# Performance work log

Hardware: AMD Instinct MI355X
Metric: run time of the kernel (lower is better)

The kernel has to match this reference:

```python
import jax, jax.numpy as jnp
import numpy as np

N, H, T, L, D_IN, D_QK, D_V = 8, 8, 1024, 1024, 128, 128, 128


def setup_inputs() -> dict:
    key = jax.random.key(0)
    ks = jax.random.split(key, 12)
    s = 1.0 / np.sqrt(D_IN)
    sq = 1.0 / np.sqrt(D_QK)
    return {
        "X": jax.random.normal(ks[0], (N, H, L, D_IN), jnp.float32),
        "t1": jax.random.normal(ks[1], (N, T), jnp.float32),
        "Q": jax.random.normal(ks[2], (N, H, T, D_QK), jnp.float32),
        "Wk1": jax.random.normal(ks[3], (D_IN, D_QK), jnp.float32) * s,
        "bk1": jnp.zeros((D_QK,), jnp.float32),
        "Wk2": jax.random.normal(ks[4], (D_QK, D_QK), jnp.float32) * sq,
        "bk2": jnp.zeros((D_QK,), jnp.float32),
        "Wv1": jax.random.normal(ks[5], (D_IN, D_QK), jnp.float32) * s,
        "bv1": jnp.zeros((D_QK,), jnp.float32),
        "Wv2": jax.random.normal(ks[6], (D_QK, D_V), jnp.float32) * sq,
        "bv2": jnp.zeros((D_V,), jnp.float32),
        "log_tau": jnp.asarray(0.0, jnp.float32),  # log(init_tau=1)
    }


def _mlp(x, W1, b1, W2, b2):
    # MLP(d_in, [d_qk], d_out): Linear -> relu -> Linear
    return jax.nn.relu(x @ W1 + b1) @ W2 + b2


def reference(X, t1, Q, Wk1, bk1, Wk2, bk2, Wv1, bv1, Wv2, bv2, log_tau):
    t2 = X[:, 0, :, -1]                      # (N, L)
    K = _mlp(X, Wk1, bk1, Wk2, bk2)          # (N, H, L, d_qk)
    V = _mlp(X, Wv1, bv1, Wv2, bv2)          # (N, H, L, d_v)
    tau = jnp.exp(log_tau)
    # gaussian weight: -(Q.K)^2 / tau
    A = jnp.einsum('nhtc,nhlc->nhtl', Q, K)
    A = -(A * A) / tau
    mask = (t1[:, :, None] >= t2[:, None, :])[:, None, :, :]  # (N,1,T,L)
    A = jax.nn.softmax(A * mask, axis=-1) * mask
    return jnp.einsum('nhtl,nhlc->nhtc', A, V)
```

## Files before the change

### kernel.cpp

```cpp
#include <hip/hip_runtime.h>
#include <hip/hip_bf16.h>

typedef __bf16 bf16_t;
typedef _Float16 f16_t;
typedef bf16_t bf16x8 __attribute__((ext_vector_type(8)));
typedef f16_t  f16x8  __attribute__((ext_vector_type(8)));
typedef f16_t  f16x4  __attribute__((ext_vector_type(4)));
typedef float  floatx4 __attribute__((ext_vector_type(4)));
typedef float  floatx16 __attribute__((ext_vector_type(16)));
typedef bf16x8 bf16x8u __attribute__((aligned(8)));

#define DEV static __device__ __forceinline__

DEV floatx4 mfma16_bf16(bf16x8 a, bf16x8 b, floatx4 c) {
  return __builtin_amdgcn_mfma_f32_16x16x32_bf16(a, b, c, 0, 0, 0);
}
DEV floatx16 mfma32_bf16(bf16x8 a, bf16x8 b, floatx16 c) {
  return __builtin_amdgcn_mfma_f32_32x32x16_bf16(a, b, c, 0, 0, 0);
}
DEV floatx16 mfma32x8_f16(f16x4 a, f16x4 b, floatx16 c) {
  return __builtin_amdgcn_mfma_f32_32x32x8f16(a, b, c, 0, 0, 0);
}
DEV void async_ld16(void* lds, const void* g) {
  __builtin_amdgcn_global_load_lds(
      (const __attribute__((address_space(1))) unsigned int*)g,
      (__attribute__((address_space(3))) unsigned int*)lds, 16, 0, 0);
}

__global__ void prep_kernel(const float* __restrict__ Wk1, const float* __restrict__ Wk2,
                            const float* __restrict__ Wv1, const float* __restrict__ Wv2,
                            const float* __restrict__ X,
                            bf16_t* __restrict__ W1p, bf16_t* __restrict__ W2p,
                            bf16_t* __restrict__ W3p, bf16_t* __restrict__ W4p,
                            float* __restrict__ t2pre) {
  int b = blockIdx.x;
  if (b < 16) {
    int m = b >> 2, p = b & 3;
    const float* src = m == 0 ? Wk1 : m == 1 ? Wk2 : m == 2 ? Wv1 : Wv2;
    bf16_t* dst = m == 0 ? W1p : m == 1 ? W2p : m == 2 ? W3p : W4p;
    for (int u = 0; u < 16; ++u) {
      int idx = p * 4096 + u * 256 + threadIdx.x;
      int k = idx >> 7, nn = idx & 127;
      float v = src[idx];
      int o = nn * 128 + k;
      bf16_t h = (bf16_t)v;
      dst[o] = h;
      dst[16384 + o] = (bf16_t)(v - (float)h);
    }
  } else {
    int i = (b - 16) * 256 + threadIdx.x;
    t2pre[i] = X[((size_t)(i >> 10) * 8192 + (i & 1023)) * 128 + 127];
  }
}

__global__ __launch_bounds__(256) void mlp_k_kernel(
    const float* __restrict__ X, const float* __restrict__ b1,
    const float* __restrict__ b2, const bf16_t* __restrict__ W1p,
    const bf16_t* __restrict__ W2p, bf16_t* __restrict__ Khi,
    bf16_t* __restrict__ Klo) {
  __shared__ __align__(16) char sXbuf[2 * 16896];
  __shared__ __align__(16) bf16_t sW[2][256 * 40];
  bf16_t* sXh = (bf16_t*)sXbuf;
  bf16_t* sXl = sXh + 64 * 132;

  const int tid = threadIdx.x, lane = tid & 63, wave = tid >> 6;
  const int q = lane >> 4, c15 = lane & 15;
  const size_t rowBase = (size_t)blockIdx.x * 64;

  int goff[5];
  for (int a = 0; a < 5; ++a) {
    int o = (wave + 4 * a) * 1024 + lane * 16;
    int row = o / 80, rem = o % 80;
    goff[a] = row * 256 + (rem < 64 ? rem : 0);
  }
  float b1v[8], b2v[8];
  for (int nt = 0; nt < 8; ++nt) { b1v[nt] = b1[nt * 16 + c15]; b2v[nt] = b2[nt * 16 + c15]; }

  for (int u = 0; u < 8; ++u) {
    int idx = tid + u * 256;
    int r = idx >> 5, c4 = (idx & 31) << 2;
    float4 v = *(const float4*)(X + (rowBase + r) * 128 + c4);
    int o = r * 132 + c4;
    float vv[4] = {v.x, v.y, v.z, v.w};
    for (int i = 0; i < 4; ++i) {
      bf16_t h = (bf16_t)vv[i];
      sXh[o + i] = h;
      sXl[o + i] = (bf16_t)(vv[i] - (float)h);
    }
  }

  auto issueW = [&](int buf, int ph) {
    const bf16_t* Wp = (ph < 4) ? W1p : W2p;
    const char* base = (const char*)Wp + (ph & 3) * 64;
    for (int a = 0; a < 5; ++a)
      async_ld16((char*)sW[buf] + (wave + 4 * a) * 1024 + lane * 16, base + goff[a]);
  };

  floatx4 acc1[8], acc2[8];
  for (int i = 0; i < 8; ++i) { acc1[i] = {}; acc2[i] = {}; }

  issueW(0, 0);
  __syncthreads();
#pragma unroll
  for (int ph = 0; ph < 8; ++ph) {
    if (ph < 7) issueW((ph + 1) & 1, ph + 1);
    const bf16_t* wb = sW[ph & 1];
    const int kq = ph & 3;
    floatx4* acc = (ph < 4) ? acc1 : acc2;
    const int ao = (wave * 16 + c15) * 132 + kq * 32 + q * 8;
    bf16x8 ah = *(const bf16x8u*)(sXh + ao);
    bf16x8 al = *(const bf16x8u*)(sXl + ao);
    for (int nt = 0; nt < 8; ++nt) {
      const int bo = (nt * 16 + c15) * 40 + q * 8;
      bf16x8 bh = *(const bf16x8*)(wb + bo);
      bf16x8 bl = *(const bf16x8*)(wb + 128 * 40 + bo);
      acc[nt] = mfma16_bf16(ah, bh, acc[nt]);
      acc[nt] = mfma16_bf16(ah, bl, acc[nt]);
      acc[nt] = mfma16_bf16(al, bh, acc[nt]);
    }
    if (ph == 3) {
      for (int nt = 0; nt < 8; ++nt)
        for (int r = 0; r < 4; ++r) {
          float h = fmaxf(acc1[nt][r] + b1v[nt], 0.f);
          bf16_t hh = (bf16_t)h;
          int o = (wave * 16 + q * 4 + r) * 132 + nt * 16 + c15;
          sXh[o] = hh;
          sXl[o] = (bf16_t)(h - (float)hh);
        }
    }
    __syncthreads();
  }

  for (int nt = 0; nt < 8; ++nt)
    for (int r = 0; r < 4; ++r) {
      float kv = acc2[nt][r] + b2v[nt];
      bf16_t kh = (bf16_t)kv;
      int o = (wave * 16 + q * 4 + r) * 132 + nt * 16 + c15;
      sXh[o] = kh;
      sXl[o] = (bf16_t)(kv - (float)kh);
    }
  __syncthreads();
  for (int u = 0; u < 4; ++u) {
    int idx = tid + u * 256;
    int r = idx >> 4, c8 = (idx & 15) << 3;
    bf16x8 vh = *(const bf16x8u*)(sXh + r * 132 + c8);
    bf16x8 vl = *(const bf16x8u*)(sXl + r * 132 + c8);
    *(bf16x8*)(Khi + (rowBase + r) * 128 + c8) = vh;
    *(bf16x8*)(Klo + (rowBase + r) * 128 + c8) = vl;
  }
}

__global__ __launch_bounds__(256) void mlp_v_kernel(
    const float* __restrict__ X, const float* __restrict__ b1,
    const float* __restrict__ b2, const bf16_t* __restrict__ W1p,
    const bf16_t* __restrict__ W2p, f16_t* __restrict__ Vt) {
  __shared__ __align__(16) char sXbuf[2 * 16896];
  __shared__ __align__(16) bf16_t sW[2][256 * 40];
  bf16_t* sXh = (bf16_t*)sXbuf;
  bf16_t* sXl = sXh + 64 * 132;

  const int tid = threadIdx.x, lane = tid & 63, wave = tid >> 6;
  const int q = lane >> 4, c15 = lane & 15;
  const size_t rowBase = (size_t)blockIdx.x * 64;

  int goff[5];
  for (int a = 0; a < 5; ++a) {
    int o = (wave + 4 * a) * 1024 + lane * 16;
    int row = o / 80, rem = o % 80;
    goff[a] = row * 256 + (rem < 64 ? rem : 0);
  }
  float b1v[8], bvv[2][4];
  for (int nt = 0; nt < 8; ++nt) b1v[nt] = b1[nt * 16 + c15];
  for (int mt = 0; mt < 2; ++mt)
    for (int r = 0; r < 4; ++r)
      bvv[mt][r] = b2[(wave * 2 + mt) * 16 + q * 4 + r];

  for (int u = 0; u < 8; ++u) {
    int idx = tid + u * 256;
    int r = idx >> 5, c4 = (idx & 31) << 2;
    float4 v = *(const float4*)(X + (rowBase + r) * 128 + c4);
    int o = r * 132 + c4;
    float vv[4] = {v.x, v.y, v.z, v.w};
    for (int i = 0; i < 4; ++i) {
      bf16_t h = (bf16_t)vv[i];
      sXh[o + i] = h;
      sXl[o + i] = (bf16_t)(vv[i] - (float)h);
    }
  }

  auto issueW = [&](int buf, int ph) {
    const bf16_t* Wp = (ph < 4) ? W1p : W2p;
    const char* base = (const char*)Wp + (ph & 3) * 64;
    for (int a = 0; a < 5; ++a)
      async_ld16((char*)sW[buf] + (wave + 4 * a) * 1024 + lane * 16, base + goff[a]);
  };

  floatx4 acc1[8], acc2[2][4];
  for (int i = 0; i < 8; ++i) acc1[i] = {};
  for (int i = 0; i < 2; ++i) for (int j = 0; j < 4; ++j) acc2[i][j] = {};

  issueW(0, 0);
  __syncthreads();
#pragma unroll
  for (int ph = 0; ph < 8; ++ph) {
    if (ph < 7) issueW((ph + 1) & 1, ph + 1);
    const bf16_t* wb = sW[ph & 1];
    const int kq = ph & 3;
    if (ph < 4) {
      const int ao = (wave * 16 + c15) * 132 + kq * 32 + q * 8;
      bf16x8 ah = *(const bf16x8u*)(sXh + ao);
      bf16x8 al = *(const bf16x8u*)(sXl + ao);
      for (int nt = 0; nt < 8; ++nt) {
        const int bo = (nt * 16 + c15) * 40 + q * 8;
        bf16x8 bh = *(const bf16x8*)(wb + bo);
        bf16x8 bl = *(const bf16x8*)(wb + 128 * 40 + bo);
        acc1[nt] = mfma16_bf16(ah, bh, acc1[nt]);
        acc1[nt] = mfma16_bf16(ah, bl, acc1[nt]);
        acc1[nt] = mfma16_bf16(al, bh, acc1[nt]);
      }
      if (ph == 3) {
        for (int nt = 0; nt < 8; ++nt)
          for (int r = 0; r < 4; ++r) {
            float h = fmaxf(acc1[nt][r] + b1v[nt], 0.f);
            bf16_t hh = (bf16_t)h;
            int o = (wave * 16 + q * 4 + r) * 132 + nt * 16 + c15;
            sXh[o] = hh;
            sXl[o] = (bf16_t)(h - (float)hh);
          }
      }
    } else {
      bf16x8 awh[2], awl[2];
      for (int mt = 0; mt < 2; ++mt) {
        const int aoo = ((wave * 2 + mt) * 16 + c15) * 40 + q * 8;
        awh[mt] = *(const bf16x8*)(wb + aoo);
        awl[mt] = *(const bf16x8*)(wb + 128 * 40 + aoo);
      }
      for (int nt = 0; nt < 4; ++nt) {
        const int bo = (nt * 16 + c15) * 132 + kq * 32 + q * 8;
        bf16x8 bh = *(const bf16x8u*)(sXh + bo);
        bf16x8 bl = *(const bf16x8u*)(sXl + bo);
        for (int mt = 0; mt < 2; ++mt) {
          acc2[mt][nt] = mfma16_bf16(awh[mt], bh, acc2[mt][nt]);
          acc2[mt][nt] = mfma16_bf16(awh[mt], bl, acc2[mt][nt]);
          acc2[mt][nt] = mfma16_bf16(awl[mt], bh, acc2[mt][nt]);
        }
      }
    }
    __syncthreads();
  }

  f16_t* sVT = (f16_t*)sXbuf;
  for (int mt = 0; mt < 2; ++mt)
    for (int nt = 0; nt < 4; ++nt)
      for (int r = 0; r < 4; ++r) {
        int c = (wave * 2 + mt) * 16 + q * 4 + r;
        sVT[c * 72 + nt * 16 + c15] = (f16_t)(acc2[mt][nt][r] + bvv[mt][r]);
      }
  __syncthreads();
  const int nh = (int)(rowBase >> 10);
  const int lB = (int)(rowBase & 1023);
  for (int u = 0; u < 4; ++u) {
    int idx = tid + u * 256;
    int c = idx >> 3, l8 = (idx & 7) << 3;
    *(f16x8*)(Vt + ((size_t)nh * 128 + c) * 1024 + lB + l8) =
        *(const f16x8*)(sVT + c * 72 + l8);
  }
}

__global__ __launch_bounds__(256, 2) void attn_kernel(
    const float* __restrict__ Q, const float* __restrict__ t1,
    const float* __restrict__ t2pre, const float* __restrict__ ltau,
    const bf16_t* __restrict__ Khi, const bf16_t* __restrict__ Klo,
    const f16_t* __restrict__ Vt, float* __restrict__ out) {
  __shared__ __align__(16) char sBuf[2][27648];
  __shared__ __align__(16) float sT2[1024];

  const int tid = threadIdx.x, lane = tid & 63, wave = tid >> 6;
  const int h = lane >> 5, l31 = lane & 31;
  const int nh = blockIdx.x & 63;
  const int tB = (blockIdx.x >> 6) << 7;
  const int n = nh >> 3;
  const int qrow = tB + wave * 32 + l31;
  const float c2 = __expf(-ltau[0]) * 1.44269504f;

  const char* gp[7]; int ls[7]; int st[7];
  for (int a = 0; a < 7; ++a) {
    int j = wave + 4 * a;
    gp[a] = nullptr; ls[a] = 0; st[a] = 0;
    if (j < 17) {
      int o = j * 1024 + lane * 16;
      int half = o >= 8704 ? 1 : 0;
      int r2 = o - half * 8704;
      int row = r2 / 272, rem = r2 % 272;
      if (rem >= 256) rem = 0;
      gp[a] = (const char*)(half ? Klo : Khi) + ((size_t)((nh << 10) + row)) * 256 + rem;
      st[a] = 8192; ls[a] = o;
    } else if (j < 27) {
      int o = (j - 17) * 1024 + lane * 16;
      int c = o / 80, rem = o % 80;
      if (rem >= 64) rem = 0;
      gp[a] = (const char*)Vt + ((size_t)((nh << 7) + c)) * 2048 + rem;
      st[a] = 64; ls[a] = 17408 + o;
    }
  }
  auto stage = [&](int buf) {
    for (int a = 0; a < 7; ++a) {
      int j = wave + 4 * a;
      if (j < 27) { async_ld16(sBuf[buf] + ls[a], gp[a]); gp[a] += st[a]; }
    }
  };

  stage(0);
  *(float4*)(sT2 + tid * 4) = *(const float4*)(t2pre + (n << 10) + tid * 4);

  bf16x8 qh[8], ql[8];
  {
    const float* qr = Q + ((size_t)(nh << 10) + qrow) * 128;
    for (int ks = 0; ks < 8; ++ks) {
      const float* p = qr + ks * 16 + h * 8;
      float4 v0 = *(const float4*)p;
      float4 v1 = *(const float4*)(p + 4);
      float vv[8] = {v0.x, v0.y, v0.z, v0.w, v1.x, v1.y, v1.z, v1.w};
      bf16x8 hi, lo;
      for (int j = 0; j < 8; ++j) {
        bf16_t hj = (bf16_t)vv[j];
        hi[j] = hj;
        lo[j] = (bf16_t)(vv[j] - (float)hj);
      }
      qh[ks] = hi;
      ql[ks] = lo;
    }
  }
  const float t1v = t1[(n << 10) + qrow];

  floatx16 O[4];
  for (int i = 0; i < 4; ++i) O[i] = {};
  float ds = 0.f;

  __syncthreads();
  for (int it = 0; it < 32; ++it) {
    const int cur = it & 1;
    if (it < 31) stage(cur ^ 1);
    const char* kb = sBuf[cur];
    const char* vb = sBuf[cur] + 17408;

    floatx16 S = {};
    for (int ks = 0; ks < 8; ++ks) {
      const int bo = l31 * 272 + ks * 32 + h * 16;
      bf16x8 kh_ = *(const bf16x8*)(kb + bo);
      bf16x8 kl_ = *(const bf16x8*)(kb + 8704 + bo);
      S = mfma32_bf16(kh_, qh[ks], S);
      S = mfma32_bf16(kl_, qh[ks], S);
      S = mfma32_bf16(kh_, ql[ks], S);
    }

    const float* t2b = sT2 + it * 32 + h * 4;
    for (int t = 0; t < 4; ++t) {
      float4 t2v = *(const float4*)(t2b + t * 8);
      float tv[4] = {t2v.x, t2v.y, t2v.z, t2v.w};
      f16x4 pb;
      for (int j = 0; j < 4; ++j) {
        float s = S[4 * t + j];
        float e = exp2f(-s * s * c2);
        bool m = (t1v >= tv[j]);
        ds += m ? e : 1.f;
        pb[j] = (f16_t)(m ? e : 0.f);
      }
      for (int ct = 0; ct < 4; ++ct) {
        f16x4 va = *(const f16x4*)(vb + (ct * 32 + l31) * 80 + t * 16 + h * 8);
        O[ct] = mfma32x8_f16(va, pb, O[ct]);
      }
    }
    __syncthreads();
  }

  ds += __shfl_xor(ds, 32);
  const float inv = 1.f / ds;
  float* orow = out + ((size_t)(nh << 10) + qrow) * 128;
  for (int ct = 0; ct < 4; ++ct)
    for (int t = 0; t < 4; ++t) {
      int c = ct * 32 + 8 * t + 4 * h;
      float4 v = {O[ct][4 * t + 0] * inv, O[ct][4 * t + 1] * inv,
                  O[ct][4 * t + 2] * inv, O[ct][4 * t + 3] * inv};
      *(float4*)(orow + c) = v;
    }
}

extern "C" void kernel_launch(void* const* d_in, const int* in_sizes, int n_in,
                              void* d_out, int out_size, void* d_ws, size_t ws_size,
                              hipStream_t stream) {
  const float* X   = (const float*)d_in[0];
  const float* t1  = (const float*)d_in[1];
  const float* Q   = (const float*)d_in[2];
  const float* Wk1 = (const float*)d_in[3];
  const float* bk1 = (const float*)d_in[4];
  const float* Wk2 = (const float*)d_in[5];
  const float* bk2 = (const float*)d_in[6];
  const float* Wv1 = (const float*)d_in[7];
  const float* bv1 = (const float*)d_in[8];
  const float* Wv2 = (const float*)d_in[9];
  const float* bv2 = (const float*)d_in[10];
  const float* log_tau = (const float*)d_in[11];
  float* out = (float*)d_out;

  const size_t E = (size_t)64 * 1024 * 128;
  bf16_t* Khi = (bf16_t*)d_ws;
  bf16_t* Klo = Khi + E;
  f16_t*  Vt  = (f16_t*)(Klo + E);
  bf16_t* W1p = (bf16_t*)((char*)d_ws + 3 * E * 2);
  bf16_t* W2p = W1p + 32768;
  bf16_t* W3p = W2p + 32768;
  bf16_t* W4p = W3p + 32768;
  float*  t2pre = (float*)(W4p + 32768);

  prep_kernel<<<48, 256, 0, stream>>>(Wk1, Wk2, Wv1, Wv2, X, W1p, W2p, W3p, W4p, t2pre);
  mlp_k_kernel<<<1024, 256, 0, stream>>>(X, bk1, bk2, W1p, W2p, Khi, Klo);
  mlp_v_kernel<<<1024, 256, 0, stream>>>(X, bv1, bv2, W3p, W4p, Vt);
  attn_kernel<<<512, 256, 0, stream>>>(Q, t1, t2pre, log_tau, Khi, Klo, Vt, out);
}
```

Before: 250.2 us.

## Use fp16 single-pass V MLP, triple-buffer attention, and widen attention blocks

```diff
diff --git a/kernel.cpp b/kernel.cpp
--- a/kernel.cpp
+++ b/kernel.cpp
@@ -9,11 +9,15 @@
 typedef float  floatx4 __attribute__((ext_vector_type(4)));
 typedef float  floatx16 __attribute__((ext_vector_type(16)));
 typedef bf16x8 bf16x8u __attribute__((aligned(8)));
+typedef f16x8  f16x8u  __attribute__((aligned(8)));
 
 #define DEV static __device__ __forceinline__
 
 DEV floatx4 mfma16_bf16(bf16x8 a, bf16x8 b, floatx4 c) {
   return __builtin_amdgcn_mfma_f32_16x16x32_bf16(a, b, c, 0, 0, 0);
+}
+DEV floatx4 mfma16_f16(f16x8 a, f16x8 b, floatx4 c) {
+  return __builtin_amdgcn_mfma_f32_16x16x32_f16(a, b, c, 0, 0, 0);
 }
 DEV floatx16 mfma32_bf16(bf16x8 a, bf16x8 b, floatx16 c) {
   return __builtin_amdgcn_mfma_f32_32x32x16_bf16(a, b, c, 0, 0, 0);
@@ -26,26 +30,55 @@
       (const __attribute__((address_space(1))) unsigned int*)g,
       (__attribute__((address_space(3))) unsigned int*)lds, 16, 0, 0);
 }
+DEV float fast_exp2(float x) {
+  float r;
+  asm("v_exp_f32 %0, %1" : "=v"(r) : "v"(x));
+  return r;
+}
 
 __global__ void prep_kernel(const float* __restrict__ Wk1, const float* __restrict__ Wk2,
                             const float* __restrict__ Wv1, const float* __restrict__ Wv2,
                             const float* __restrict__ X,
                             bf16_t* __restrict__ W1p, bf16_t* __restrict__ W2p,
-                            bf16_t* __restrict__ W3p, bf16_t* __restrict__ W4p,
+                            f16_t* __restrict__ W3f, f16_t* __restrict__ W4f,
                             float* __restrict__ t2pre) {
   int b = blockIdx.x;
   if (b < 16) {
     int m = b >> 2, p = b & 3;
     const float* src = m == 0 ? Wk1 : m == 1 ? Wk2 : m == 2 ? Wv1 : Wv2;
-    bf16_t* dst = m == 0 ? W1p : m == 1 ? W2p : m == 2 ? W3p : W4p;
-    for (int u = 0; u < 16; ++u) {
-      int idx = p * 4096 + u * 256 + threadIdx.x;
-      int k = idx >> 7, nn = idx & 127;
-      float v = src[idx];
-      int o = nn * 128 + k;
-      bf16_t h = (bf16_t)v;
-      dst[o] = h;
-      dst[16384 + o] = (bf16_t)(v - (float)h);
+    __shared__ float tile[32][129];
+    for (int u = 0; u < 4; ++u) {
+      int idx = threadIdx.x + u * 256;
+      int k = idx >> 5, n4 = (idx & 31) << 2;
+      float4 v = *(const float4*)(src + (size_t)(p * 32 + k) * 128 + n4);
+      tile[k][n4 + 0] = v.x; tile[k][n4 + 1] = v.y;
+      tile[k][n4 + 2] = v.z; tile[k][n4 + 3] = v.w;
+    }
+    __syncthreads();
+    if (m < 2) {
+      bf16_t* dst = m ? W2p : W1p;
+      for (int u = 0; u < 2; ++u) {
+        int idx = threadIdx.x + u * 256;
+        int n = idx >> 2, kc = idx & 3;
+        bf16x8 hi, lo;
+        for (int j = 0; j < 8; ++j) {
+          float v = tile[kc * 8 + j][n];
+          bf16_t hh = (bf16_t)v;
+          hi[j] = hh;
+          lo[j] = (bf16_t)(v - (float)hh);
+        }
+        *(bf16x8*)(dst + n * 128 + p * 32 + kc * 8) = hi;
+        *(bf16x8*)(dst + 16384 + n * 128 + p * 32 + kc * 8) = lo;
+      }
+    } else {
+      f16_t* dst = (m == 3) ? W4f : W3f;
+      for (int u = 0; u < 2; ++u) {
+        int idx = threadIdx.x + u * 256;
+        int n = idx >> 2, kc = idx & 3;
+        f16x8 w;
+        for (int j = 0; j < 8; ++j) w[j] = (f16_t)tile[kc * 8 + j][n];
+        *(f16x8*)(dst + n * 128 + p * 32 + kc * 8) = w;
+      }
     }
   } else {
     int i = (b - 16) * 256 + threadIdx.x;
@@ -73,6 +106,15 @@
     int row = o / 80, rem = o % 80;
     goff[a] = row * 256 + (rem < 64 ? rem : 0);
   }
+  auto issueW = [&](int buf, int ph) {
+    const bf16_t* Wp = (ph < 4) ? W1p : W2p;
+    const char* base = (const char*)Wp + (ph & 3) * 64;
+    for (int a = 0; a < 5; ++a)
+      async_ld16((char*)sW[buf] + (wave + 4 * a) * 1024 + lane * 16, base + goff[a]);
+  };
+
+  issueW(0, 0);
+
   float b1v[8], b2v[8];
   for (int nt = 0; nt < 8; ++nt) { b1v[nt] = b1[nt * 16 + c15]; b2v[nt] = b2[nt * 16 + c15]; }
 
@@ -89,17 +131,9 @@
     }
   }
 
-  auto issueW = [&](int buf, int ph) {
-    const bf16_t* Wp = (ph < 4) ? W1p : W2p;
-    const char* base = (const char*)Wp + (ph & 3) * 64;
-    for (int a = 0; a < 5; ++a)
-      async_ld16((char*)sW[buf] + (wave + 4 * a) * 1024 + lane * 16, base + goff[a]);
-  };
-
   floatx4 acc1[8], acc2[8];
   for (int i = 0; i < 8; ++i) { acc1[i] = {}; acc2[i] = {}; }
 
-  issueW(0, 0);
   __syncthreads();
 #pragma unroll
   for (int ph = 0; ph < 8; ++ph) {
@@ -152,23 +186,32 @@
 
 __global__ __launch_bounds__(256) void mlp_v_kernel(
     const float* __restrict__ X, const float* __restrict__ b1,
-    const float* __restrict__ b2, const bf16_t* __restrict__ W1p,
-    const bf16_t* __restrict__ W2p, f16_t* __restrict__ Vt) {
-  __shared__ __align__(16) char sXbuf[2 * 16896];
-  __shared__ __align__(16) bf16_t sW[2][256 * 40];
-  bf16_t* sXh = (bf16_t*)sXbuf;
-  bf16_t* sXl = sXh + 64 * 132;
+    const float* __restrict__ b2, const f16_t* __restrict__ W1f,
+    const f16_t* __restrict__ W2f, f16_t* __restrict__ Vt) {
+  __shared__ __align__(16) f16_t sXf[64 * 136];
+  __shared__ __align__(16) f16_t sW[2][128 * 40];
 
   const int tid = threadIdx.x, lane = tid & 63, wave = tid >> 6;
   const int q = lane >> 4, c15 = lane & 15;
   const size_t rowBase = (size_t)blockIdx.x * 64;
 
-  int goff[5];
-  for (int a = 0; a < 5; ++a) {
+  int goff[3];
+  for (int a = 0; a < 3; ++a) {
     int o = (wave + 4 * a) * 1024 + lane * 16;
     int row = o / 80, rem = o % 80;
     goff[a] = row * 256 + (rem < 64 ? rem : 0);
   }
+  auto issueV = [&](int buf, int ph) {
+    const f16_t* Wp = (ph < 4) ? W1f : W2f;
+    const char* base = (const char*)Wp + (ph & 3) * 64;
+    for (int a = 0; a < 3; ++a) {
+      int j = wave + 4 * a;
+      if (j < 10) async_ld16((char*)sW[buf] + j * 1024 + lane * 16, base + goff[a]);
+    }
+  };
+
+  issueV(0, 0);
+
   float b1v[8], bvv[2][4];
   for (int nt = 0; nt < 8; ++nt) b1v[nt] = b1[nt * 16 + c15];
   for (int mt = 0; mt < 2; ++mt)
@@ -179,82 +222,51 @@
     int idx = tid + u * 256;
     int r = idx >> 5, c4 = (idx & 31) << 2;
     float4 v = *(const float4*)(X + (rowBase + r) * 128 + c4);
-    int o = r * 132 + c4;
-    float vv[4] = {v.x, v.y, v.z, v.w};
-    for (int i = 0; i < 4; ++i) {
-      bf16_t h = (bf16_t)vv[i];
-      sXh[o + i] = h;
-      sXl[o + i] = (bf16_t)(vv[i] - (float)h);
-    }
-  }
-
-  auto issueW = [&](int buf, int ph) {
-    const bf16_t* Wp = (ph < 4) ? W1p : W2p;
-    const char* base = (const char*)Wp + (ph & 3) * 64;
-    for (int a = 0; a < 5; ++a)
-      async_ld16((char*)sW[buf] + (wave + 4 * a) * 1024 + lane * 16, base + goff[a]);
-  };
+    int o = r * 136 + c4;
+    sXf[o + 0] = (f16_t)v.x; sXf[o + 1] = (f16_t)v.y;
+    sXf[o + 2] = (f16_t)v.z; sXf[o + 3] = (f16_t)v.w;
+  }
 
   floatx4 acc1[8], acc2[2][4];
   for (int i = 0; i < 8; ++i) acc1[i] = {};
   for (int i = 0; i < 2; ++i) for (int j = 0; j < 4; ++j) acc2[i][j] = {};
 
-  issueW(0, 0);
   __syncthreads();
 #pragma unroll
   for (int ph = 0; ph < 8; ++ph) {
-    if (ph < 7) issueW((ph + 1) & 1, ph + 1);
-    const bf16_t* wb = sW[ph & 1];
+    if (ph < 7) issueV((ph + 1) & 1, ph + 1);
+    const f16_t* wb = sW[ph & 1];
     const int kq = ph & 3;
     if (ph < 4) {
-      const int ao = (wave * 16 + c15) * 132 + kq * 32 + q * 8;
-      bf16x8 ah = *(const bf16x8u*)(sXh + ao);
-      bf16x8 al = *(const bf16x8u*)(sXl + ao);
+      f16x8 a = *(const f16x8u*)(sXf + (wave * 16 + c15) * 136 + kq * 32 + q * 8);
       for (int nt = 0; nt < 8; ++nt) {
-        const int bo = (nt * 16 + c15) * 40 + q * 8;
-        bf16x8 bh = *(const bf16x8*)(wb + bo);
-        bf16x8 bl = *(const bf16x8*)(wb + 128 * 40 + bo);
-        acc1[nt] = mfma16_bf16(ah, bh, acc1[nt]);
-        acc1[nt] = mfma16_bf16(ah, bl, acc1[nt]);
-        acc1[nt] = mfma16_bf16(al, bh, acc1[nt]);
+        f16x8 bb = *(const f16x8*)(wb + (nt * 16 + c15) * 40 + q * 8);
+        acc1[nt] = mfma16_f16(a, bb, acc1[nt]);
       }
       if (ph == 3) {
         for (int nt = 0; nt < 8; ++nt)
-          for (int r = 0; r < 4; ++r) {
-            float h = fmaxf(acc1[nt][r] + b1v[nt], 0.f);
-            bf16_t hh = (bf16_t)h;
-            int o = (wave * 16 + q * 4 + r) * 132 + nt * 16 + c15;
-            sXh[o] = hh;
-            sXl[o] = (bf16_t)(h - (float)hh);
-          }
+          for (int r = 0; r < 4; ++r)
+            sXf[(wave * 16 + q * 4 + r) * 136 + nt * 16 + c15] =
+                (f16_t)fmaxf(acc1[nt][r] + b1v[nt], 0.f);
       }
     } else {
-      bf16x8 awh[2], awl[2];
-      for (int mt = 0; mt < 2; ++mt) {
-        const int aoo = ((wave * 2 + mt) * 16 + c15) * 40 + q * 8;
-        awh[mt] = *(const bf16x8*)(wb + aoo);
-        awl[mt] = *(const bf16x8*)(wb + 128 * 40 + aoo);
-      }
+      f16x8 aw0 = *(const f16x8*)(wb + ((wave * 2 + 0) * 16 + c15) * 40 + q * 8);
+      f16x8 aw1 = *(const f16x8*)(wb + ((wave * 2 + 1) * 16 + c15) * 40 + q * 8);
       for (int nt = 0; nt < 4; ++nt) {
-        const int bo = (nt * 16 + c15) * 132 + kq * 32 + q * 8;
-        bf16x8 bh = *(const bf16x8u*)(sXh + bo);
-        bf16x8 bl = *(const bf16x8u*)(sXl + bo);
-        for (int mt = 0; mt < 2; ++mt) {
-          acc2[mt][nt] = mfma16_bf16(awh[mt], bh, acc2[mt][nt]);
-          acc2[mt][nt] = mfma16_bf16(awh[mt], bl, acc2[mt][nt]);
-          acc2[mt][nt] = mfma16_bf16(awl[mt], bh, acc2[mt][nt]);
-        }
+        f16x8 bh = *(const f16x8u*)(sXf + (nt * 16 + c15) * 136 + kq * 32 + q * 8);
+        acc2[0][nt] = mfma16_f16(aw0, bh, acc2[0][nt]);
+        acc2[1][nt] = mfma16_f16(aw1, bh, acc2[1][nt]);
       }
     }
     __syncthreads();
   }
 
-  f16_t* sVT = (f16_t*)sXbuf;
+  f16_t* sVT = sXf;
   for (int mt = 0; mt < 2; ++mt)
     for (int nt = 0; nt < 4; ++nt)
       for (int r = 0; r < 4; ++r) {
         int c = (wave * 2 + mt) * 16 + q * 4 + r;
-        sVT[c * 72 + nt * 16 + c15] = (f16_t)(acc2[mt][nt][r] + bvv[mt][r]);
+        sVT[c * 68 + nt * 16 + c15] = (f16_t)(acc2[mt][nt][r] + bvv[mt][r]);
       }
   __syncthreads();
   const int nh = (int)(rowBase >> 10);
@@ -263,30 +275,30 @@
     int idx = tid + u * 256;
     int c = idx >> 3, l8 = (idx & 7) << 3;
     *(f16x8*)(Vt + ((size_t)nh * 128 + c) * 1024 + lB + l8) =
-        *(const f16x8*)(sVT + c * 72 + l8);
-  }
-}
-
-__global__ __launch_bounds__(256, 2) void attn_kernel(
+        *(const f16x8u*)(sVT + c * 68 + l8);
+  }
+}
+
+__global__ __launch_bounds__(512, 2) void attn_kernel(
     const float* __restrict__ Q, const float* __restrict__ t1,
     const float* __restrict__ t2pre, const float* __restrict__ ltau,
     const bf16_t* __restrict__ Khi, const bf16_t* __restrict__ Klo,
     const f16_t* __restrict__ Vt, float* __restrict__ out) {
-  __shared__ __align__(16) char sBuf[2][27648];
+  __shared__ __align__(16) char sBuf[3][27648];
   __shared__ __align__(16) float sT2[1024];
 
   const int tid = threadIdx.x, lane = tid & 63, wave = tid >> 6;
   const int h = lane >> 5, l31 = lane & 31;
   const int nh = blockIdx.x & 63;
-  const int tB = (blockIdx.x >> 6) << 7;
+  const int tB = (blockIdx.x >> 6) << 8;
   const int n = nh >> 3;
   const int qrow = tB + wave * 32 + l31;
-  const float c2 = __expf(-ltau[0]) * 1.44269504f;
-
-  const char* gp[7]; int ls[7]; int st[7];
-  for (int a = 0; a < 7; ++a) {
-    int j = wave + 4 * a;
-    gp[a] = nullptr; ls[a] = 0; st[a] = 0;
+  const float negc2 = -__expf(-ltau[0]) * 1.44269504f;
+
+  const char* gp[4]; int ls[4]; int st[4];
+  for (int a = 0; a < 4; ++a) {
+    int j = wave + 8 * a;
+    if (j >= 27) j -= 5;
     if (j < 17) {
       int o = j * 1024 + lane * 16;
       int half = o >= 8704 ? 1 : 0;
@@ -295,7 +307,7 @@
       if (rem >= 256) rem = 0;
       gp[a] = (const char*)(half ? Klo : Khi) + ((size_t)((nh << 10) + row)) * 256 + rem;
       st[a] = 8192; ls[a] = o;
-    } else if (j < 27) {
+    } else {
       int o = (j - 17) * 1024 + lane * 16;
       int c = o / 80, rem = o % 80;
       if (rem >= 64) rem = 0;
@@ -304,15 +316,11 @@
     }
   }
   auto stage = [&](int buf) {
-    for (int a = 0; a < 7; ++a) {
-      int j = wave + 4 * a;
-      if (j < 27) { async_ld16(sBuf[buf] + ls[a], gp[a]); gp[a] += st[a]; }
-    }
+    for (int a = 0; a < 4; ++a) { async_ld16(sBuf[buf] + ls[a], gp[a]); gp[a] += st[a]; }
   };
 
-  stage(0);
-  *(float4*)(sT2 + tid * 4) = *(const float4*)(t2pre + (n << 10) + tid * 4);
-
+  float2 t2v2 = *(const float2*)(t2pre + (n << 10) + tid * 2);
+  const float t1v = t1[(n << 10) + qrow];
   bf16x8 qh[8], ql[8];
   {
     const float* qr = Q + ((size_t)(nh << 10) + qrow) * 128;
@@ -331,18 +339,22 @@
       ql[ks] = lo;
     }
   }
-  const float t1v = t1[(n << 10) + qrow];
+  stage(0);
+  stage(1);
+  *(float2*)(sT2 + tid * 2) = t2v2;
 
   floatx16 O[4];
   for (int i = 0; i < 4; ++i) O[i] = {};
   float ds = 0.f;
 
-  __syncthreads();
+  asm volatile("s_waitcnt vmcnt(4) lgkmcnt(0)" ::: "memory");
+  __builtin_amdgcn_s_barrier();
+  asm volatile("" ::: "memory");
+
   for (int it = 0; it < 32; ++it) {
-    const int cur = it & 1;
-    if (it < 31) stage(cur ^ 1);
-    const char* kb = sBuf[cur];
-    const char* vb = sBuf[cur] + 17408;
+    if (it < 30) stage((it + 2) % 3);
+    const char* kb = sBuf[it % 3];
+    const char* vb = kb + 17408;
 
     floatx16 S = {};
     for (int ks = 0; ks < 8; ++ks) {
@@ -356,12 +368,12 @@
 
     const float* t2b = sT2 + it * 32 + h * 4;
     for (int t = 0; t < 4; ++t) {
-      float4 t2v = *(const float4*)(t2b + t * 8);
-      float tv[4] = {t2v.x, t2v.y, t2v.z, t2v.w};
+      float4 tv4 = *(const float4*)(t2b + t * 8);
+      float tv[4] = {tv4.x, tv4.y, tv4.z, tv4.w};
       f16x4 pb;
       for (int j = 0; j < 4; ++j) {
         float s = S[4 * t + j];
-        float e = exp2f(-s * s * c2);
+        float e = fast_exp2(s * s * negc2);
         bool m = (t1v >= tv[j]);
         ds += m ? e : 1.f;
         pb[j] = (f16_t)(m ? e : 0.f);
@@ -371,7 +383,17 @@
         O[ct] = mfma32x8_f16(va, pb, O[ct]);
       }
     }
-    __syncthreads();
+
+    if (it < 30) {
+      asm volatile("s_waitcnt vmcnt(4)" ::: "memory");
+    } else if (it == 30) {
+      asm volatile("s_waitcnt vmcnt(0)" ::: "memory");
+    }
+    if (it < 31) {
+      asm volatile("" ::: "memory");
+      __builtin_amdgcn_s_barrier();
+      asm volatile("" ::: "memory");
+    }
   }
 
   ds += __shfl_xor(ds, 32);
@@ -409,12 +431,12 @@
   f16_t*  Vt  = (f16_t*)(Klo + E);
   bf16_t* W1p = (bf16_t*)((char*)d_ws + 3 * E * 2);
   bf16_t* W2p = W1p + 32768;
-  bf16_t* W3p = W2p + 32768;
-  bf16_t* W4p = W3p + 32768;
-  float*  t2pre = (float*)(W4p + 32768);
-
-  prep_kernel<<<48, 256, 0, stream>>>(Wk1, Wk2, Wv1, Wv2, X, W1p, W2p, W3p, W4p, t2pre);
+  f16_t*  W3f = (f16_t*)(W2p + 32768);
+  f16_t*  W4f = W3f + 16384;
+  float*  t2pre = (float*)(W4f + 16384);
+
+  prep_kernel<<<48, 256, 0, stream>>>(Wk1, Wk2, Wv1, Wv2, X, W1p, W2p, W3f, W4f, t2pre);
   mlp_k_kernel<<<1024, 256, 0, stream>>>(X, bk1, bk2, W1p, W2p, Khi, Klo);
-  mlp_v_kernel<<<1024, 256, 0, stream>>>(X, bv1, bv2, W3p, W4p, Vt);
-  attn_kernel<<<512, 256, 0, stream>>>(Q, t1, t2pre, log_tau, Khi, Klo, Vt, out);
-}
+  mlp_v_kernel<<<1024, 256, 0, stream>>>(X, bv1, bv2, W3f, W4f, Vt);
+  attn_kernel<<<256, 512, 0, stream>>>(Q, t1, t2pre, log_tau, Khi, Klo, Vt, out);
+}
```

After: 234.9 us. 1.07x faster.
